# Performance work log

Measured on AMD Instinct MI355X. Metric: run time of the kernel, lower is better.

Reference implementation:

```python
import math
import jax, jax.numpy as jnp
import numpy as np

SR = 44100
N_HARMONICS = 64
EPS = 1e-5
LOG10 = math.log(10.0)


def scale_function(x):
    # ddsp_pytorch util.scale_function: 2 * sigmoid(x)**log(10) + 1e-7
    return 2.0 * jax.nn.sigmoid(x) ** LOG10 + 1e-7


def setup_inputs() -> dict:
    key = jax.random.key(0)
    k1, k2, k3 = jax.random.split(key, 3)
    bs, n_samples = 32, 64000
    # f0 in [80, 480] Hz so upper harmonics cross Nyquist for some frames
    f0_hz = jax.random.uniform(k1, (bs, n_samples), dtype=jnp.float32) * 400.0 + 80.0
    harmonic_amplitudes = jax.random.normal(k2, (bs, n_samples, N_HARMONICS + 1), dtype=jnp.float32)
    phase = jax.random.uniform(k3, (bs,), dtype=jnp.float32) * 2.0 * jnp.pi
    return {"f0_hz": f0_hz, "harmonic_amplitudes": harmonic_amplitudes, "phase": phase}


def reference(f0_hz, harmonic_amplitudes, phase):
    ha = scale_function(harmonic_amplitudes)            # (bs, S, H+1)
    f0 = f0_hz[..., None]                               # (bs, S, 1)
    total_amplitude = ha[..., :1]                       # (bs, S, 1)
    ha = ha[..., 1:]                                    # (bs, S, H)
    harm = jnp.arange(1, N_HARMONICS + 1, dtype=f0.dtype)  # (H,)
    # anti-alias: zero harmonics above Nyquist
    aa = (f0 * harm < SR / 2).astype(f0.dtype)
    ha_aa = ha * aa
    ha_aa = ha_aa / (jnp.sum(ha_aa, axis=-1, keepdims=True) + EPS)
    ha_aa = ha_aa * total_amplitude
    # phase integration
    omega = jnp.cumsum(2.0 * jnp.pi * f0 / SR, axis=1)  # (bs, S, 1)
    omega = omega + phase.reshape(-1, 1, 1)
    omegas = omega * harm                               # (bs, S, H)
    signal = jnp.sum(jnp.sin(omegas) * ha_aa, axis=-1)  # (bs, S)
    return signal
```

## Files before the change

### kernel.cpp

```cpp
#include <hip/hip_runtime.h>
#include <math.h>

#define N_SAMP   64000
#define BATCH    32
#define CHUNK    128
#define NCHUNK   500
#define NH       64

__global__ __launch_bounds__(128) void chunk_sum_kernel(
        const float* __restrict__ f0, double* __restrict__ csum) {
    int bx = blockIdx.x;
    int t  = threadIdx.x;
    double v = (double)f0[(long)bx * CHUNK + t];
    for (int off = 32; off > 0; off >>= 1) v += __shfl_down(v, off, 64);
    __shared__ double ws[2];
    if ((t & 63) == 0) ws[t >> 6] = v;
    __syncthreads();
    if (t == 0) csum[bx] = ws[0] + ws[1];
}

__global__ __launch_bounds__(512) void chunk_scan_kernel(double* __restrict__ csum) {
    int r = blockIdx.x;
    int t = threadIdx.x;
    int lane = t & 63, w = t >> 6;
    double orig = (t < NCHUNK) ? csum[(long)r * NCHUNK + t] : 0.0;
    double v = orig;
    for (int off = 1; off < 64; off <<= 1) {
        double n = __shfl_up(v, off, 64);
        if (lane >= off) v += n;
    }
    __shared__ double wsum[8];
    if (lane == 63) wsum[w] = v;
    __syncthreads();
    double add = 0.0;
    for (int i = 0; i < w; ++i) add += wsum[i];
    v += add;
    if (t < NCHUNK) csum[(long)r * NCHUNK + t] = v - orig;
}

__device__ __forceinline__ float scale_fn(float x) {
    float e = exp2f(-1.4426950408889634f * x);
    float l = log2f(1.0f + e);
    return 2.0f * exp2f(-2.302585092994046f * l) + 1e-7f;
}

__global__ __launch_bounds__(128) void osc_kernel(
        const float* __restrict__ f0,
        const float* __restrict__ ha,
        const float* __restrict__ phase,
        const double* __restrict__ csum,
        float* __restrict__ out) {
    int bx = blockIdx.x;
    int r  = bx / NCHUNK;
    int t  = threadIdx.x;
    int lane = t & 63, w = t >> 6;

    long sbase = (long)bx * CHUNK;
    const float* hablk = ha + sbase * 65;

    __shared__ float amp[CHUNK * 65];
    {
        const float4* src = (const float4*)hablk;
        float4* dst = (float4*)amp;
        #pragma unroll
        for (int i = 0; i < 16; ++i)
            dst[i * 128 + t] = src[i * 128 + t];
        if (t < 2080 - 16 * 128)
            dst[16 * 128 + t] = src[16 * 128 + t];
    }

    float f0v = f0[sbase + t];

    double v = (double)f0v;
    for (int off = 1; off < 64; off <<= 1) {
        double n = __shfl_up(v, off, 64);
        if (lane >= off) v += n;
    }
    __shared__ double wsum[2];
    if (lane == 63) wsum[w] = v;
    __syncthreads();
    if (w == 1) v += wsum[0];
    v += csum[bx];
    double x = v * (1.0 / 44100.0) + (double)phase[r] * 0.15915494309189535;
    x -= floor(x);
    float nu = (float)x;

    float traw = amp[t * 65];
    float S1 = 0.0f, S2 = 0.0f;
    const float half_sr = 22050.0f;
    #pragma unroll 16
    for (int h = 0; h < 64; ++h) {
        float hf = (float)(h + 1);
        float a  = amp[t * 65 + 1 + h];
        float wv = scale_fn(a);
        wv = (f0v * hf < half_sr) ? wv : 0.0f;
        float t1 = nu * hf;
        float fr = t1 - floorf(t1);
        float sv = __sinf(6.283185307179586f * fr);
        S1 += wv;
        S2 = fmaf(wv, sv, S2);
    }

    out[sbase + t] = scale_fn(traw) * S2 / (S1 + 1e-5f);
}

extern "C" void kernel_launch(void* const* d_in, const int* in_sizes, int n_in,
                              void* d_out, int out_size, void* d_ws, size_t ws_size,
                              hipStream_t stream) {
    const float* f0    = (const float*)d_in[0];
    const float* ha    = (const float*)d_in[1];
    const float* phase = (const float*)d_in[2];
    float* out = (float*)d_out;
    double* csum = (double*)d_ws;

    chunk_sum_kernel<<<BATCH * NCHUNK, CHUNK, 0, stream>>>(f0, csum);
    chunk_scan_kernel<<<BATCH, 512, 0, stream>>>(csum);
    osc_kernel<<<BATCH * NCHUNK, CHUNK, 0, stream>>>(f0, ha, phase, csum, out);
}
```

Measured before the change: 719.7 us.

## Replace per-harmonic sigmoid-power with LUT and sine recurrence

Each harmonic's scale_function (exp2/log2/exp2) is replaced by a linearly interpolated lookup table of 1152 entries over [-8, 10], built by a small kernel and staged into shared memory per block. The per-harmonic sin is replaced by an angle-addition recurrence from one sin/cos pair. The Nyquist mask becomes a precomputed harmonic cutoff k0. This cuts transcendental work in the inner loop, but the table clamps inputs outside its range and interpolates, and the recurrence accumulates rounding error across 64 harmonics, so accuracy may drift.

```diff
diff --git a/kernel.cpp b/kernel.cpp
--- a/kernel.cpp
+++ b/kernel.cpp
@@ -1,11 +1,21 @@
 #include <hip/hip_runtime.h>
 #include <math.h>
 
-#define N_SAMP   64000
 #define BATCH    32
 #define CHUNK    128
 #define NCHUNK   500
-#define NH       64
+#define TAB_N    1152
+
+__device__ __forceinline__ float scale_fn(float x) {
+    float e = exp2f(-1.4426950408889634f * x);
+    float l = log2f(1.0f + e);
+    return 2.0f * exp2f(-2.302585092994046f * l) + 1e-7f;
+}
+
+__global__ __launch_bounds__(128) void table_kernel(float* __restrict__ gtab) {
+    int i = blockIdx.x * 128 + threadIdx.x;
+    if (i < TAB_N) gtab[i] = scale_fn(fmaf((float)i, 0.015625f, -8.0f));
+}
 
 __global__ __launch_bounds__(128) void chunk_sum_kernel(
         const float* __restrict__ f0, double* __restrict__ csum) {
@@ -38,17 +48,12 @@
     if (t < NCHUNK) csum[(long)r * NCHUNK + t] = v - orig;
 }
 
-__device__ __forceinline__ float scale_fn(float x) {
-    float e = exp2f(-1.4426950408889634f * x);
-    float l = log2f(1.0f + e);
-    return 2.0f * exp2f(-2.302585092994046f * l) + 1e-7f;
-}
-
 __global__ __launch_bounds__(128) void osc_kernel(
         const float* __restrict__ f0,
         const float* __restrict__ ha,
         const float* __restrict__ phase,
         const double* __restrict__ csum,
+        const float* __restrict__ gtab,
         float* __restrict__ out) {
     int bx = blockIdx.x;
     int r  = bx / NCHUNK;
@@ -59,13 +64,22 @@
     const float* hablk = ha + sbase * 65;
 
     __shared__ float amp[CHUNK * 65];
+    __shared__ float tab[TAB_N];
+
+    {
+        const float4* ts = (const float4*)gtab;
+        float4* td = (float4*)tab;
+        td[t]       = ts[t];
+        td[t + 128] = ts[t + 128];
+        if (t < 32) td[t + 256] = ts[t + 256];
+    }
     {
         const float4* src = (const float4*)hablk;
         float4* dst = (float4*)amp;
         #pragma unroll
         for (int i = 0; i < 16; ++i)
             dst[i * 128 + t] = src[i * 128 + t];
-        if (t < 2080 - 16 * 128)
+        if (t < 32)
             dst[16 * 128 + t] = src[16 * 128 + t];
     }
 
@@ -85,23 +99,37 @@
     x -= floor(x);
     float nu = (float)x;
 
-    float traw = amp[t * 65];
+    float k0 = floorf(22050.0f / f0v);
+    if (f0v * (k0 + 1.0f) < 22050.0f)      k0 += 1.0f;
+    else if (!(f0v * k0 < 22050.0f))       k0 -= 1.0f;
+
+    float th = 6.283185307179586f * nu;
+    float s1 = __sinf(th);
+    float c1 = __cosf(th);
+    float s = s1, c = c1;
+
     float S1 = 0.0f, S2 = 0.0f;
-    const float half_sr = 22050.0f;
-    #pragma unroll 16
+    #pragma unroll 8
     for (int h = 0; h < 64; ++h) {
-        float hf = (float)(h + 1);
         float a  = amp[t * 65 + 1 + h];
-        float wv = scale_fn(a);
-        wv = (f0v * hf < half_sr) ? wv : 0.0f;
-        float t1 = nu * hf;
-        float fr = t1 - floorf(t1);
-        float sv = __sinf(6.283185307179586f * fr);
+        float tc = fmaf(a, 64.0f, 512.0f);
+        tc = fminf(fmaxf(tc, 0.0f), 1022.99f);
+        float fi = floorf(tc);
+        int   i  = (int)fi;
+        float fr = tc - fi;
+        float w0 = tab[i];
+        float w1 = tab[i + 1];
+        float wv = fmaf(fr, w1 - w0, w0);
+        wv = ((float)(h + 1) <= k0) ? wv : 0.0f;
         S1 += wv;
-        S2 = fmaf(wv, sv, S2);
+        S2 = fmaf(wv, s, S2);
+        float ns = fmaf(s, c1,  c * s1);
+        float nc = fmaf(c, c1, -(s * s1));
+        s = ns; c = nc;
     }
 
-    out[sbase + t] = scale_fn(traw) * S2 / (S1 + 1e-5f);
+    float total = scale_fn(amp[t * 65]);
+    out[sbase + t] = total * S2 / (S1 + 1e-5f);
 }
 
 extern "C" void kernel_launch(void* const* d_in, const int* in_sizes, int n_in,
@@ -111,9 +139,12 @@
     const float* ha    = (const float*)d_in[1];
     const float* phase = (const float*)d_in[2];
     float* out = (float*)d_out;
+
     double* csum = (double*)d_ws;
+    float*  gtab = (float*)((char*)d_ws + 131072);
 
+    table_kernel<<<(TAB_N + 127) / 128, 128, 0, stream>>>(gtab);
     chunk_sum_kernel<<<BATCH * NCHUNK, CHUNK, 0, stream>>>(f0, csum);
     chunk_scan_kernel<<<BATCH, 512, 0, stream>>>(csum);
-    osc_kernel<<<BATCH * NCHUNK, CHUNK, 0, stream>>>(f0, ha, phase, csum, out);
+    osc_kernel<<<BATCH * NCHUNK, CHUNK, 0, stream>>>(f0, ha, phase, csum, gtab, out);
 }
```

Measured after the change: 697.4 us. 1.03x faster.
